# Kernel optimization log

Measured on AMD Instinct MI355X. Metric: run time of the kernel, lower is better.

The kernel has to match this reference:

```python
import jax, jax.numpy as jnp
import numpy as np

HEADS, DIM_HEADS = 16, 16
SCALE = DIM_HEADS ** -0.5

# (forward_perm, inverse_perm) for each axial dim of x: (B, S, E, H, W)
# axial axes are 1 (seq), 3 (H=4), 4 (W=5); emb axis 2 moved to last, axial axis to second-last
_PERMS = [
    ((0, 3, 4, 1, 2), (0, 3, 4, 1, 2)),  # seq axis (self-inverse)
    ((0, 1, 4, 3, 2), (0, 1, 4, 3, 2)),  # H axis (self-inverse)
    ((0, 1, 3, 4, 2), (0, 1, 4, 2, 3)),  # W axis
]


def _self_attn(x, wq, wkv, wo_w, wo_b):
    # x: (..., t, d); standard multi-head self-attention along t
    q = x @ wq.T                               # (..., t, 256)
    k, v = jnp.split(x @ wkv.T, 2, axis=-1)    # each (..., t, 256)
    lead, tlen = x.shape[:-2], x.shape[-2]
    sh = (*lead, tlen, HEADS, DIM_HEADS)
    q, k, v = q.reshape(sh), k.reshape(sh), v.reshape(sh)
    scores = jnp.einsum('...thd,...shd->...hts', q, k) * SCALE
    attn = jax.nn.softmax(scores, axis=-1)
    o = jnp.einsum('...hts,...shd->...thd', attn, v)
    o = o.reshape(*lead, tlen, HEADS * DIM_HEADS)
    return o @ wo_w.T + wo_b


def _axial_attention_layer(x, wq_l, wkv_l, wo_w_l, wo_b_l):
    # sum of attention along each axial dim (sum_axial_out=True)
    out = jnp.zeros_like(x)
    for a, (p, ip) in enumerate(_PERMS):
        y = jnp.transpose(x, p)
        y = _self_attn(y, wq_l[a], wkv_l[a], wo_w_l[a], wo_b_l[a])
        out = out + jnp.transpose(y, ip)
    return out


def setup_inputs() -> dict:
    key = jax.random.key(0)
    ks = jax.random.split(key, 8)
    B, S, E, H, W = 32, 64, 256, 4, 5
    return {
        'x': jax.random.normal(ks[0], (B, S, E, H, W), jnp.float32),
        'pos_s': jax.random.normal(ks[1], (1, S, E, 1, 1), jnp.float32),
        'pos_h': jax.random.normal(ks[2], (1, 1, E, H, 1), jnp.float32),
        'pos_w': jax.random.normal(ks[3], (1, 1, E, 1, W), jnp.float32),
        'wq': jax.random.normal(ks[4], (2, 3, 256, E), jnp.float32) * 0.02,
        'wkv': jax.random.normal(ks[5], (2, 3, 512, E), jnp.float32) * 0.02,
        'wo_w': jax.random.normal(ks[6], (2, 3, E, 256), jnp.float32) * 0.02,
        'wo_b': jnp.zeros((2, 3, E), jnp.float32),
        'dec_w': jax.random.normal(ks[7], (1, E), jnp.float32) * 0.02,
        'dec_b': jnp.zeros((1,), jnp.float32),
    }


def reference(x, pos_s, pos_h, pos_w, wq, wkv, wo_w, wo_b, dec_w, dec_b):
    # additive axial positional embeddings
    x = x + pos_s + pos_h + pos_w
    # two stacked AxialAttention blocks (no residual in the wrapper)
    for l in range(2):
        x = _axial_attention_layer(x, wq[l], wkv[l], wo_w[l], wo_b[l])
    # (B, S, E, H, W) -> (B, S, H, W, E), linear decode to 1 channel, sigmoid
    x = jnp.transpose(x, (0, 1, 3, 4, 2))
    return jax.nn.sigmoid(x @ dec_w.T + dec_b)
```

## Files before the change

### kernel.cpp

```cpp
#include <hip/hip_runtime.h>
#include <stdint.h>

typedef unsigned short u16;
typedef u16 u16x8 __attribute__((ext_vector_type(8)));
typedef __bf16 bf16x8 __attribute__((ext_vector_type(8)));
typedef float f32x4 __attribute__((ext_vector_type(4)));
typedef float f32x16 __attribute__((ext_vector_type(16)));

#define NE   256
#define NPOS 40960
#define QLD  2304

__device__ __forceinline__ float bf2f(u16 h) {
  union { unsigned u; float f; } c; c.u = ((unsigned)h) << 16; return c.f;
}
__device__ __forceinline__ u16 f2bf(float f) {
  union { float f; unsigned u; } c; c.f = f;
  unsigned u = c.u;
  return (u16)((u + 0x7FFFu + ((u >> 16) & 1u)) >> 16);
}
__device__ __forceinline__ unsigned pkbf(float a, float b) {
  unsigned r;
  asm("v_cvt_pk_bf16_f32 %0, %1, %2" : "=v"(r) : "v"(a), "v"(b));
  return r;
}
__device__ __forceinline__ void gll16(const void* g, void* l) {
  __builtin_amdgcn_global_load_lds(
      (const __attribute__((address_space(1))) void*)g,
      (__attribute__((address_space(3))) void*)l, 16, 0, 0);
}
template<int N> __device__ __forceinline__ void waitvm() {
  if constexpr (N == 0)       asm volatile("s_waitcnt vmcnt(0)"  ::: "memory");
  else if constexpr (N == 2)  asm volatile("s_waitcnt vmcnt(2)"  ::: "memory");
  else if constexpr (N == 4)  asm volatile("s_waitcnt vmcnt(4)"  ::: "memory");
  else if constexpr (N == 8)  asm volatile("s_waitcnt vmcnt(8)"  ::: "memory");
}

#define PK_T1 (6*768*256)
#define PK_T2 (2*256*768)
#define PREP_BLK 2048
#define PACK_BLK ((PK_T1 + PK_T2 + 512) / 256)
__global__ __launch_bounds__(256) void prep_pack(
    const float* __restrict__ x, const float* __restrict__ pos_s,
    const float* __restrict__ pos_h, const float* __restrict__ pos_w,
    u16* __restrict__ xb,
    const float* __restrict__ wq, const float* __restrict__ wkv,
    const float* __restrict__ wo, const float* __restrict__ wo_b,
    u16* __restrict__ wqp, u16* __restrict__ wop, float* __restrict__ bsum)
{
  __shared__ float Ls[256 * 21];
  const int tid = threadIdx.x;
  if (blockIdx.x < PREP_BLK) {
    const int bs = blockIdx.x;
    const int s  = bs & 63;
    const float* xp = x + (size_t)bs * 5120;
    for (int i = tid; i < 5120; i += 256) {
      int e = i / 20, hw = i % 20;
      int h = hw / 5, w = hw % 5;
      float v = xp[i] + pos_s[s * 256 + e] + pos_h[e * 4 + h] + pos_w[e * 5 + w];
      Ls[e * 21 + hw] = v;
    }
    __syncthreads();
    u16* op = xb + (size_t)bs * 20 * 256;
    for (int i = tid; i < 5120; i += 256) {
      int nl = i >> 8, e = i & 255;
      op[nl * 256 + e] = f2bf(Ls[e * 21 + nl]);
    }
  } else {
    int i = (blockIdx.x - PREP_BLK) * 256 + tid;
    if (i < PK_T1) {
      int la = i / (768 * 256);
      int rem = i - la * (768 * 256);
      int r = rem >> 8, c = rem & 255;
      float v = (r < 256) ? wq[(size_t)la * 65536 + r * 256 + c] * 0.25f
                          : wkv[(size_t)la * 131072 + (r - 256) * 256 + c];
      wqp[i] = f2bf(v);
    } else if (i < PK_T1 + PK_T2) {
      int j = i - PK_T1;
      int l = j / 196608;
      int rem = j - l * 196608;
      int out = rem / 768, k = rem % 768;
      int a = k >> 8, in = k & 255;
      wop[j] = f2bf(wo[(size_t)(((l * 3 + a) * 256) + out) * 256 + in]);
    } else if (i < PK_T1 + PK_T2 + 512) {
      int j = i - PK_T1 - PK_T2;
      int l = j >> 8, c = j & 255;
      bsum[j] = wo_b[(l * 3 + 0) * 256 + c] + wo_b[(l * 3 + 1) * 256 + c]
              + wo_b[(l * 3 + 2) * 256 + c];
    }
  }
}

template<int NKT, int NBN, int TPB>
__global__ __launch_bounds__(256, 2) void gemm_stream(
    const u16* __restrict__ A, const u16* __restrict__ B,
    u16* __restrict__ Cb, int ldc)
{
  constexpr int K     = NKT * 32;
  constexpr int NSTEP = NKT * TPB;
  __shared__ alignas(16) u16 Bs[128 * K];
  __shared__ alignas(16) u16 As[2][128 * 32];

  const int nblk = gridDim.x;
  const int bid  = blockIdx.x;
  const int mapped = (bid & 7) * (nblk >> 3) + (bid >> 3);
  const int strip = mapped / NBN, bn = mapped % NBN;
  const int bm0 = strip * TPB;

  const int tid  = threadIdx.x;
  const int lane = tid & 63, w = tid >> 6;
  const int wr   = (w >> 1) * 64, wc = (w & 1) * 64;
  const int r16  = lane & 15, khi = lane >> 4;
  const int pofs = (khi ^ ((r16 >> 1) & 3)) * 8;

  const u16* gB = B + (size_t)bn * 128 * K;
  const u16* gA = A + (size_t)bm0 * 128 * K;

  #pragma unroll
  for (int b = 0; b < K / 16; ++b) {
    int slot = tid + b * 256;
    int kt = slot >> 9, rem = slot & 511;
    int row = rem >> 2, c = rem & 3;
    int cs = c ^ ((row >> 1) & 3);
    gll16(gB + (size_t)row * K + kt * 32 + cs * 8, (char*)Bs + slot * 16);
  }

  auto STAGE_A = [&](int g) {
    const int t = g / NKT, kt = g % NKT;
    const u16* tA = gA + (size_t)t * 128 * K + kt * 32;
    u16* dst = As[g & 1];
    #pragma unroll
    for (int r = 0; r < 2; ++r) {
      int i = tid + r * 256;
      int row = i >> 2, s = i & 3;
      int ss = s ^ ((row >> 1) & 3);
      gll16(tA + (size_t)row * K + ss * 8, (char*)dst + i * 16);
    }
  };

  f32x4 acc[4][4] = {};
  STAGE_A(0);

  for (int t = 0; t < TPB; ++t) {
    #pragma unroll
    for (int kt = 0; kt < NKT; ++kt) {
      const int g = t * NKT + kt;
      __builtin_amdgcn_s_barrier();
      if (g + 1 < NSTEP) { STAGE_A(g + 1); waitvm<2>(); }
      else               { waitvm<0>(); }
      asm volatile("" ::: "memory");

      const u16* Ab = As[g & 1];
      const u16* Bk = Bs + kt * (128 * 32);
      bf16x8 af[4], bfr[4];
      #pragma unroll
      for (int m = 0; m < 4; ++m)
        af[m] = *(const bf16x8*)(Ab + (wr + m * 16 + r16) * 32 + pofs);
      #pragma unroll
      for (int n = 0; n < 4; ++n)
        bfr[n] = *(const bf16x8*)(Bk + (wc + n * 16 + r16) * 32 + pofs);
      __builtin_amdgcn_s_setprio(1);
      #pragma unroll
      for (int m = 0; m < 4; ++m)
        #pragma unroll
        for (int n = 0; n < 4; ++n)
          acc[m][n] = __builtin_amdgcn_mfma_f32_16x16x32_bf16(af[m], bfr[n], acc[m][n], 0, 0, 0);
      __builtin_amdgcn_s_setprio(0);
      asm volatile("" ::: "memory");
    }
    const int row0 = (bm0 + t) * 128 + wr + khi * 4;
    const int col0 = bn * 128 + wc + r16;
    #pragma unroll
    for (int m = 0; m < 4; ++m)
      #pragma unroll
      for (int n = 0; n < 4; ++n)
        #pragma unroll
        for (int j = 0; j < 4; ++j) {
          Cb[(size_t)(row0 + m * 16 + j) * ldc + col0 + n * 16] = f2bf(acc[m][n][j]);
          acc[m][n][j] = 0.f;
        }
  }
}

template<int MODE, int NKT, int NBN>
__global__ __launch_bounds__(256, 2) void gemm_bt(
    const u16* __restrict__ A, const u16* __restrict__ B,
    u16* __restrict__ Cb, const float* __restrict__ bias,
    const float* __restrict__ dw, float* __restrict__ logit,
    int ldc)
{
  constexpr int K   = NKT * 32;
  constexpr int TSZ = 256 * 32;
  __shared__ alignas(16) u16 smem[3 * TSZ];

  const int bid = blockIdx.x;
  const int cpx = gridDim.x >> 3;
  const int mapped = (bid & 7) * cpx + (bid >> 3);
  const int bm = mapped / NBN, bn = mapped % NBN;

  const int tid  = threadIdx.x;
  const int lane = tid & 63, w = tid >> 6;
  const int wr   = (w >> 1) * 64, wc = (w & 1) * 64;
  const int r16  = lane & 15, khi = lane >> 4;
  const int pofs = (khi ^ ((r16 >> 1) & 3)) * 8;

  f32x4 acc[4][4] = {};

  const u16* gA = A + (size_t)bm * 128 * QLD;
  const u16* gB = B + (size_t)bn * 128 * K;

  auto STAGE = [&](int kt, int which) {
    u16* As = smem + which * TSZ;
    u16* Bsl = As + 128 * 32;
    #pragma unroll
    for (int r = 0; r < 2; ++r) {
      int i = tid + r * 256;
      int row = i >> 2, s = i & 3;
      int col = kt * 32 + (s ^ ((row >> 1) & 3)) * 8;
      int phys = (col >> 8) * 768 + (col & 255);
      gll16(gA + (size_t)row * QLD + phys, (char*)As + i * 16);
    }
    #pragma unroll
    for (int r = 0; r < 2; ++r) {
      int i = tid + r * 256;
      int row = i >> 2, s = i & 3;
      int ss = s ^ ((row >> 1) & 3);
      gll16(gB + (size_t)row * K + kt * 32 + ss * 8, (char*)Bsl + i * 16);
    }
  };

  STAGE(0, 0);
  STAGE(1, 1);
  #pragma unroll
  for (int kt = 0; kt < NKT; ++kt) {
    const int cur = kt % 3;
    if (kt + 2 < NKT)      { STAGE(kt + 2, (kt + 2) % 3); waitvm<8>(); }
    else if (kt + 1 < NKT) { waitvm<4>(); }
    else                   { waitvm<0>(); }
    __builtin_amdgcn_s_barrier();
    asm volatile("" ::: "memory");

    const u16* As = smem + cur * TSZ;
    const u16* Bsl = As + 128 * 32;
    bf16x8 af[4], bfr[4];
    #pragma unroll
    for (int m = 0; m < 4; ++m)
      af[m] = *(const bf16x8*)(As + (wr + m * 16 + r16) * 32 + pofs);
    #pragma unroll
    for (int n = 0; n < 4; ++n)
      bfr[n] = *(const bf16x8*)(Bsl + (wc + n * 16 + r16) * 32 + pofs);
    __builtin_amdgcn_s_setprio(1);
    #pragma unroll
    for (int m = 0; m < 4; ++m)
      #pragma unroll
      for (int n = 0; n < 4; ++n)
        acc[m][n] = __builtin_amdgcn_mfma_f32_16x16x32_bf16(af[m], bfr[n], acc[m][n], 0, 0, 0);
    __builtin_amdgcn_s_setprio(0);

    asm volatile("" ::: "memory");
    __builtin_amdgcn_s_barrier();
  }

  const int row0 = bm * 128 + wr + khi * 4;
  const int col0 = bn * 128 + wc + r16;

  if constexpr (MODE == 4) {
    float dwv[4], bvv[4];
    #pragma unroll
    for (int n = 0; n < 4; ++n) {
      int c = col0 + n * 16;
      dwv[n] = dw[c];
      bvv[n] = bias[c];
    }
    #pragma unroll
    for (int m = 0; m < 4; ++m) {
      #pragma unroll
      for (int j = 0; j < 4; ++j) {
        float p = 0.f;
        #pragma unroll
        for (int n = 0; n < 4; ++n) p += (acc[m][n][j] + bvv[n]) * dwv[n];
        p += __shfl_xor(p, 1);
        p += __shfl_xor(p, 2);
        p += __shfl_xor(p, 4);
        p += __shfl_xor(p, 8);
        if (r16 == 0) atomicAdd(&logit[row0 + m * 16 + j], p);
      }
    }
  } else {
    #pragma unroll
    for (int m = 0; m < 4; ++m) {
      #pragma unroll
      for (int n = 0; n < 4; ++n) {
        int c = col0 + n * 16;
        float bv = bias[c];
        #pragma unroll
        for (int j = 0; j < 4; ++j) {
          int r = row0 + m * 16 + j;
          Cb[(size_t)r * ldc + c] = f2bf(acc[m][n][j] + bv);
        }
      }
    }
  }
}

template<int T>
__device__ __forceinline__ void attn1(
    u16* __restrict__ Qb, int n, int base, int stp, int hd)
{
  u16* qp = Qb + (size_t)n * QLD + hd * 16;
  u16x8 q0 = *(const u16x8*)(qp), q1 = *(const u16x8*)(qp + 8);
  float q[16];
  #pragma unroll
  for (int d = 0; d < 8; ++d) { q[d] = bf2f(q0[d]); q[d + 8] = bf2f(q1[d]); }

  float s[T];
  float m = -1e30f;
  #pragma unroll
  for (int j = 0; j < T; ++j) {
    const u16* kp = Qb + (size_t)(base + j * stp) * QLD + 256 + hd * 16;
    u16x8 k0 = *(const u16x8*)(kp), k1 = *(const u16x8*)(kp + 8);
    float a = 0.f;
    #pragma unroll
    for (int d = 0; d < 8; ++d) a += q[d] * bf2f(k0[d]) + q[d + 8] * bf2f(k1[d]);
    s[j] = a;
    m = fmaxf(m, a);
  }
  float sum = 0.f;
  float o[16];
  #pragma unroll
  for (int d = 0; d < 16; ++d) o[d] = 0.f;
  #pragma unroll
  for (int j = 0; j < T; ++j) {
    float pj = __expf(s[j] - m);
    sum += pj;
    const u16* vp = Qb + (size_t)(base + j * stp) * QLD + 512 + hd * 16;
    u16x8 w0 = *(const u16x8*)(vp), w1 = *(const u16x8*)(vp + 8);
    #pragma unroll
    for (int d = 0; d < 8; ++d) { o[d] += pj * bf2f(w0[d]); o[d + 8] += pj * bf2f(w1[d]); }
  }
  float inv = 1.0f / sum;
  u16x8 r0, r1;
  #pragma unroll
  for (int d = 0; d < 8; ++d) { r0[d] = f2bf(o[d] * inv); r1[d] = f2bf(o[d + 8] * inv); }
  *(u16x8*)(qp)     = r0;
  *(u16x8*)(qp + 8) = r1;
}

__global__ __launch_bounds__(256) void attn_all(u16* __restrict__ QKV)
{
  if (blockIdx.x < 2560) {
    const int w = threadIdx.x >> 6, lane = threadIdx.x & 63;
    const int wid = blockIdx.x * 4 + w;
    const int hd = wid & 15, g = wid >> 4;
    const int gb = g / 20, gr = g % 20;
    const int nbase = gb * 1280 + gr;
    const int lo = lane & 31, hi = lane >> 5;

    bf16x8 kf[2], qf[2];
    #pragma unroll
    for (int t = 0; t < 2; ++t) {
      size_t r = (size_t)(nbase + (lo + 32 * t) * 20) * QLD;
      kf[t] = *(const bf16x8*)(QKV + r + 256 + hd * 16 + hi * 8);
      qf[t] = *(const bf16x8*)(QKV + r +       hd * 16 + hi * 8);
    }
    union { u16 a[8]; bf16x8 v; } vt[4];
    #pragma unroll
    for (int c = 0; c < 4; ++c)
      #pragma unroll
      for (int j = 0; j < 8; ++j)
        vt[c].a[j] = QKV[(size_t)(nbase + (c * 16 + hi * 8 + j) * 20) * QLD
                         + 512 + hd * 16 + lo];

    f32x16 s00 = {}, s10 = {}, s01 = {}, s11 = {};
    s00 = __builtin_amdgcn_mfma_f32_32x32x16_bf16(kf[0], qf[0], s00, 0, 0, 0);
    s10 = __builtin_amdgcn_mfma_f32_32x32x16_bf16(kf[1], qf[0], s10, 0, 0, 0);
    s01 = __builtin_amdgcn_mfma_f32_32x32x16_bf16(kf[0], qf[1], s01, 0, 0, 0);
    s11 = __builtin_amdgcn_mfma_f32_32x32x16_bf16(kf[1], qf[1], s11, 0, 0, 0);

    auto run_qt = [&](f32x16 t0, f32x16 t1, int qt) {
      float m = -1e30f;
      #pragma unroll
      for (int r = 0; r < 16; ++r) { m = fmaxf(m, t0[r]); m = fmaxf(m, t1[r]); }
      m = fmaxf(m, __shfl_xor(m, 32));
      const float C = 1.4426950408889634f;
      float mc = m * C;
      float sum = 0.f;
      #pragma unroll
      for (int r = 0; r < 16; ++r) {
        float p0 = __builtin_amdgcn_exp2f(t0[r] * C - mc);
        float p1 = __builtin_amdgcn_exp2f(t1[r] * C - mc);
        t0[r] = p0; t1[r] = p1; sum += p0; sum += p1;
      }
      sum += __shfl_xor(sum, 32);
      float inv = __builtin_amdgcn_rcpf(sum);
      #pragma unroll
      for (int r = 0; r < 16; ++r) { t0[r] *= inv; t1[r] *= inv; }

      f32x16 oa = {};
      #pragma unroll
      for (int c = 0; c < 4; ++c) {
        const int rb = 8 * (c & 1);
        const f32x16& tt = (c < 2) ? t0 : t1;
        unsigned X0 = pkbf(tt[rb + 0], tt[rb + 1]);
        unsigned X1 = pkbf(tt[rb + 2], tt[rb + 3]);
        unsigned Y0 = pkbf(tt[rb + 4], tt[rb + 5]);
        unsigned Y1 = pkbf(tt[rb + 6], tt[rb + 7]);
        unsigned X0p = __shfl_xor((int)X0, 32), X1p = __shfl_xor((int)X1, 32);
        unsigned Y0p = __shfl_xor((int)Y0, 32), Y1p = __shfl_xor((int)Y1, 32);
        union { unsigned u[4]; bf16x8 v; } pf;
        pf.u[0] = hi ? Y0p : X0;
        pf.u[1] = hi ? Y1p : X1;
        pf.u[2] = hi ? Y0  : X0p;
        pf.u[3] = hi ? Y1  : X1p;
        oa = __builtin_amdgcn_mfma_f32_32x32x16_bf16(vt[c].v, pf.v, oa, 0, 0, 0);
      }
      unsigned P0 = pkbf(oa[0], oa[1]);
      unsigned P1 = pkbf(oa[2], oa[3]);
      unsigned P2 = pkbf(oa[4], oa[5]);
      unsigned P3 = pkbf(oa[6], oa[7]);
      unsigned sP0 = __shfl_xor((int)P0, 32), sP1 = __shfl_xor((int)P1, 32);
      unsigned sP2 = __shfl_xor((int)P2, 32), sP3 = __shfl_xor((int)P3, 32);
      union { unsigned u[4]; u16x8 v; } ov;
      ov.u[0] = hi ? sP2 : P0;
      ov.u[1] = hi ? sP3 : P1;
      ov.u[2] = hi ? P2  : sP0;
      ov.u[3] = hi ? P3  : sP1;
      u16* po = QKV + (size_t)(nbase + (qt * 32 + lo) * 20) * QLD + hd * 16 + hi * 8;
      *(u16x8*)po = ov.v;
    };
    run_qt(s00, s10, 0);
    run_qt(s01, s11, 1);
  } else {
    const int tg = (blockIdx.x - 2560) * 256 + threadIdx.x;
    const int hd = tg & 15, n = tg >> 4;
    int h  = (n % 20) / 5;
    int w5 = n % 5;
    attn1<4>(QKV + 768,  n, n - h * 5, 5, hd);
    attn1<5>(QKV + 1536, n, n - w5,    1, hd);
  }
}

__global__ __launch_bounds__(256) void sigmoid_kernel(
    const float* __restrict__ logit, const float* __restrict__ dec_b,
    float* __restrict__ out)
{
  int i = blockIdx.x * 256 + threadIdx.x;
  out[i] = 1.0f / (1.0f + __expf(-(logit[i] + dec_b[0])));
}

extern "C" void kernel_launch(void* const* d_in, const int* in_sizes, int n_in,
                              void* d_out, int out_size, void* d_ws, size_t ws_size,
                              hipStream_t stream) {
  const float* x     = (const float*)d_in[0];
  const float* pos_s = (const float*)d_in[1];
  const float* pos_h = (const float*)d_in[2];
  const float* pos_w = (const float*)d_in[3];
  const float* wq    = (const float*)d_in[4];
  const float* wkv   = (const float*)d_in[5];
  const float* wo_w  = (const float*)d_in[6];
  const float* wo_b  = (const float*)d_in[7];
  const float* dec_w = (const float*)d_in[8];
  const float* dec_b = (const float*)d_in[9];
  float* out = (float*)d_out;

  char* ws = (char*)d_ws;
  u16*   xb    = (u16*)ws;
  u16*   QKV   = (u16*)(ws + 20971520);
  u16*   wqp   = (u16*)(ws + 209715200);
  u16*   wop   = (u16*)(ws + 212074496);
  float* bsum  = (float*)(ws + 212860928);
  float* logit = (float*)(ws + 212862976);

  prep_pack<<<PREP_BLK + PACK_BLK, 256, 0, stream>>>(
      x, pos_s, pos_h, pos_w, xb, wq, wkv, wo_w, wo_b, wqp, wop, bsum);
  hipMemsetAsync(logit, 0, NPOS * sizeof(float), stream);

  for (int l = 0; l < 2; ++l) {
    gemm_stream<8, 18, 4><<<1440, 256, 0, stream>>>(
        xb, wqp + (size_t)(l * 3) * 196608, QKV, QLD);
    attn_all<<<5120, 256, 0, stream>>>(QKV);
    if (l == 0)
      gemm_bt<3, 24, 2><<<640, 256, 0, stream>>>(
          QKV, wop, xb, bsum, nullptr, nullptr, 256);
    else
      gemm_bt<4, 24, 2><<<640, 256, 0, stream>>>(
          QKV, wop + 196608, nullptr, bsum + 256, dec_w, logit, 0);
  }

  sigmoid_kernel<<<NPOS / 256, 256, 0, stream>>>(logit, dec_b, out);
}
```

Measured before the change: 313.1 us.

## Load A fragments directly from global into registers with triple buffering in gemm_stream

The stream GEMM no longer stages A tiles through LDS with async global-to-LDS loads and per-step barriers. Each wave now loads its A fragments straight from global memory into a three-deep register ring, prefetching two steps ahead, while B stays resident in LDS. This removes the LDS round trip and the per-k-step barrier for A. In exchange it uses more registers, fully unrolls the step loop, and issues global loads that are less coalesced (16-byte per-lane strided rows), which may cost occupancy or bandwidth.

After: 389.2 us. 1.24x slower.

```diff
diff --git a/kernel.cpp b/kernel.cpp
--- a/kernel.cpp
+++ b/kernel.cpp
@@ -31,7 +31,6 @@
 }
 template<int N> __device__ __forceinline__ void waitvm() {
   if constexpr (N == 0)       asm volatile("s_waitcnt vmcnt(0)"  ::: "memory");
-  else if constexpr (N == 2)  asm volatile("s_waitcnt vmcnt(2)"  ::: "memory");
   else if constexpr (N == 4)  asm volatile("s_waitcnt vmcnt(4)"  ::: "memory");
   else if constexpr (N == 8)  asm volatile("s_waitcnt vmcnt(8)"  ::: "memory");
 }
@@ -99,7 +98,6 @@
   constexpr int K     = NKT * 32;
   constexpr int NSTEP = NKT * TPB;
   __shared__ alignas(16) u16 Bs[128 * K];
-  __shared__ alignas(16) u16 As[2][128 * 32];
 
   const int nblk = gridDim.x;
   const int bid  = blockIdx.x;
@@ -114,7 +112,6 @@
   const int pofs = (khi ^ ((r16 >> 1) & 3)) * 8;
 
   const u16* gB = B + (size_t)bn * 128 * K;
-  const u16* gA = A + (size_t)bm0 * 128 * K;
 
   #pragma unroll
   for (int b = 0; b < K / 16; ++b) {
@@ -125,60 +122,55 @@
     gll16(gB + (size_t)row * K + kt * 32 + cs * 8, (char*)Bs + slot * 16);
   }
 
-  auto STAGE_A = [&](int g) {
+  const u16* aBase = A + ((size_t)bm0 * 128 + wr + r16) * K + khi * 8;
+
+  waitvm<0>();
+  __builtin_amdgcn_s_barrier();
+
+  f32x4 acc[4][4] = {};
+  bf16x8 apre[3][4];
+
+  auto LDA = [&](int g, int buf) {
     const int t = g / NKT, kt = g % NKT;
-    const u16* tA = gA + (size_t)t * 128 * K + kt * 32;
-    u16* dst = As[g & 1];
-    #pragma unroll
-    for (int r = 0; r < 2; ++r) {
-      int i = tid + r * 256;
-      int row = i >> 2, s = i & 3;
-      int ss = s ^ ((row >> 1) & 3);
-      gll16(tA + (size_t)row * K + ss * 8, (char*)dst + i * 16);
-    }
+    const u16* p = aBase + (size_t)t * 128 * K + kt * 32;
+    #pragma unroll
+    for (int m = 0; m < 4; ++m)
+      apre[buf][m] = *(const bf16x8*)(p + (size_t)m * 16 * K);
   };
 
-  f32x4 acc[4][4] = {};
-  STAGE_A(0);
-
-  for (int t = 0; t < TPB; ++t) {
-    #pragma unroll
-    for (int kt = 0; kt < NKT; ++kt) {
-      const int g = t * NKT + kt;
-      __builtin_amdgcn_s_barrier();
-      if (g + 1 < NSTEP) { STAGE_A(g + 1); waitvm<2>(); }
-      else               { waitvm<0>(); }
-      asm volatile("" ::: "memory");
-
-      const u16* Ab = As[g & 1];
-      const u16* Bk = Bs + kt * (128 * 32);
-      bf16x8 af[4], bfr[4];
-      #pragma unroll
-      for (int m = 0; m < 4; ++m)
-        af[m] = *(const bf16x8*)(Ab + (wr + m * 16 + r16) * 32 + pofs);
+  LDA(0, 0);
+  LDA(1, 1);
+
+  #pragma unroll
+  for (int g = 0; g < NSTEP; ++g) {
+    if (g + 2 < NSTEP) LDA(g + 2, (g + 2) % 3);
+    const int kt = g % NKT;
+    const u16* Bk = Bs + kt * (128 * 32);
+    bf16x8 bfr[4];
+    #pragma unroll
+    for (int n = 0; n < 4; ++n)
+      bfr[n] = *(const bf16x8*)(Bk + (wc + n * 16 + r16) * 32 + pofs);
+    #pragma unroll
+    for (int m = 0; m < 4; ++m)
       #pragma unroll
       for (int n = 0; n < 4; ++n)
-        bfr[n] = *(const bf16x8*)(Bk + (wc + n * 16 + r16) * 32 + pofs);
-      __builtin_amdgcn_s_setprio(1);
+        acc[m][n] = __builtin_amdgcn_mfma_f32_16x16x32_bf16(
+            apre[g % 3][m], bfr[n], acc[m][n], 0, 0, 0);
+
+    if (kt == NKT - 1) {
+      const int t = g / NKT;
+      const int row0 = (bm0 + t) * 128 + wr + khi * 4;
+      const int col0 = bn * 128 + wc + r16;
       #pragma unroll
       for (int m = 0; m < 4; ++m)
         #pragma unroll
         for (int n = 0; n < 4; ++n)
-          acc[m][n] = __builtin_amdgcn_mfma_f32_16x16x32_bf16(af[m], bfr[n], acc[m][n], 0, 0, 0);
-      __builtin_amdgcn_s_setprio(0);
-      asm volatile("" ::: "memory");
-    }
-    const int row0 = (bm0 + t) * 128 + wr + khi * 4;
-    const int col0 = bn * 128 + wc + r16;
-    #pragma unroll
-    for (int m = 0; m < 4; ++m)
-      #pragma unroll
-      for (int n = 0; n < 4; ++n)
-        #pragma unroll
-        for (int j = 0; j < 4; ++j) {
-          Cb[(size_t)(row0 + m * 16 + j) * ldc + col0 + n * 16] = f2bf(acc[m][n][j]);
-          acc[m][n][j] = 0.f;
-        }
+          #pragma unroll
+          for (int j = 0; j < 4; ++j) {
+            Cb[(size_t)(row0 + m * 16 + j) * ldc + col0 + n * 16] = f2bf(acc[m][n][j]);
+            acc[m][n][j] = 0.f;
+          }
+    }
   }
 }
 
```
